# Kernel optimization log

Hardware: AMD Instinct MI355X
Metric: run time of the kernel (lower is better)

The kernel has to match this reference:

```python
import jax, jax.numpy as jnp
import numpy as np
from jax import lax

# Static problem dims (match input_specs)
B, N, F, H, C = 128, 512, 512, 256, 10
EPG = 8192            # edges per graph
K1, K2 = 256, 128      # pooling_ratio=0.5 applied twice
LAMB = 1.0
BN_EPS = 1e-5


def setup_inputs() -> dict:
    key = jax.random.key(0)
    ks = jax.random.split(key, 24)
    x = jax.random.normal(ks[0], (B * N, F), dtype=jnp.float32)
    offs = (jnp.arange(B, dtype=jnp.int32) * N)[:, None]
    src = jax.random.randint(ks[1], (B, EPG), 0, N, dtype=jnp.int32) + offs
    dst = jax.random.randint(ks[2], (B, EPG), 0, N, dtype=jnp.int32) + offs
    edge_index = jnp.stack([src.reshape(-1), dst.reshape(-1)])
    batch = jnp.repeat(jnp.arange(B, dtype=jnp.int32), N)
    s = 0.05
    p = {
        'W1': jax.random.normal(ks[3], (F, H)) * s, 'b1': jnp.zeros((H,)),
        'W2': jax.random.normal(ks[4], (H, H)) * s, 'b2': jnp.zeros((H,)),
        'W3': jax.random.normal(ks[5], (H, H)) * s, 'b3': jnp.zeros((H,)),
        'att1': jax.random.normal(ks[6], (H, 2)) * s,
        'att2': jax.random.normal(ks[7], (H, 2)) * s,
        'bn_gamma': jnp.ones((H,)), 'bn_beta': jnp.zeros((H,)),
        'bn_mean': jnp.zeros((H,)), 'bn_var': jnp.ones((H,)),
        'lin1_w': jax.random.normal(ks[8], (2 * H, H)) * s, 'lin1_b': jnp.zeros((H,)),
        'lin2_w': jax.random.normal(ks[9], (H, H // 2)) * s, 'lin2_b': jnp.zeros((H // 2,)),
        'lin3_w': jax.random.normal(ks[10], (H // 2, C)) * s, 'lin3_b': jnp.zeros((C,)),
    }
    return {'x': x, 'edge_index': edge_index, 'batch': batch, **p}


def gcn_sparse(x, src, dst, W, b):
    """GCNConv: D^-1/2 (A+I) D^-1/2 X W + b over an edge list."""
    n = x.shape[0]
    loop = jnp.arange(n, dtype=src.dtype)
    s = jnp.concatenate([src, loop])
    d = jnp.concatenate([dst, loop])
    deg = jax.ops.segment_sum(jnp.ones_like(d, jnp.float32), d, num_segments=n)
    dinv = lax.rsqrt(jnp.maximum(deg, 1.0))
    xw = x @ W
    msg = xw[s] * (dinv[s] * dinv[d])[:, None]
    return jax.ops.segment_sum(msg, d, num_segments=n) + b


def structure_learn(x_sel, A_ind, att):
    # GAT-style additive attention over all node pairs within each pooled graph,
    # biased by lamb * induced adjacency, row-softmax normalized (dense HGPSL path).
    e = x_sel @ att[:, 0]              # [B,k]
    f = x_sel @ att[:, 1]              # [B,k]
    logits = e[:, :, None] + f[:, None, :] + LAMB * A_ind
    return jax.nn.softmax(logits, axis=-1)


def pool_sparse(x, src, dst, att, k_out):
    """HGPSL pool on the sparse input graph -> dense pooled graphs [B,k,k]."""
    n = x.shape[0]
    deg = jnp.maximum(jax.ops.segment_sum(jnp.ones_like(dst, jnp.float32), dst, num_segments=n), 1.0)
    neigh = jax.ops.segment_sum(x[src], dst, num_segments=n)
    score = jnp.abs(x - neigh / deg[:, None]).sum(-1)          # node information score ||(I - D^-1 A)X||_1
    _, idx = lax.top_k(score.reshape(B, N), k_out)              # [B,k]
    offs = (jnp.arange(B, dtype=jnp.int32) * N)[:, None]
    perm = (idx.astype(jnp.int32) + offs).reshape(-1)
    x_sel = x[perm].reshape(B, k_out, -1)
    # induced adjacency among selected nodes (scatter into k+1 dummy slot)
    rank = jnp.full((B * N,), -1, jnp.int32).at[perm].set(jnp.tile(jnp.arange(k_out, dtype=jnp.int32), B))
    g = src // N
    ns, nd = rank[src], rank[dst]
    valid = (ns >= 0) & (nd >= 0)
    A = jnp.zeros((B, k_out + 1, k_out + 1), jnp.float32)
    A = A.at[g, jnp.where(valid, ns, k_out), jnp.where(valid, nd, k_out)].set(1.0)
    A_ind = A[:, :k_out, :k_out]
    return x_sel, structure_learn(x_sel, A_ind, att)


def pool_dense(x, adj, att, k_out):
    deg = jnp.maximum(adj.sum(-1), 1e-9)
    prop = jnp.einsum('bij,bjf->bif', adj, x) / deg[..., None]
    score = jnp.abs(x - prop).sum(-1)                           # [B,k_in]
    _, idx = lax.top_k(score, k_out)
    x_sel = jnp.take_along_axis(x, idx[:, :, None], axis=1)
    A_ind = jax.vmap(lambda a, i: a[i][:, i])(adj, idx)
    return x_sel, structure_learn(x_sel, A_ind, att)


def gcn_dense(x, adj, W, b):
    k = x.shape[1]
    A = adj + jnp.eye(k, dtype=x.dtype)
    dinv = lax.rsqrt(A.sum(-1))
    An = A * dinv[:, :, None] * dinv[:, None, :]
    return jnp.einsum('bij,bjf->bif', An, x @ W) + b


def readout(x):
    # [gmp || gap] over nodes of each graph
    return jnp.concatenate([x.max(axis=1), x.mean(axis=1)], axis=-1)


def reference(x, edge_index, batch, W1, b1, W2, b2, W3, b3, att1, att2,
              bn_gamma, bn_beta, bn_mean, bn_var,
              lin1_w, lin1_b, lin2_w, lin2_b, lin3_w, lin3_b):
    src, dst = edge_index[0], edge_index[1]
    h = jax.nn.relu(gcn_sparse(x, src, dst, W1, b1))            # conv1, [B*N, H]
    x__ = h
    h1, adj1 = pool_sparse(h, src, dst, att1, K1)                # pool1 -> [B,K1,H]
    x1 = readout(h1)
    hb = (h1 - bn_mean) * lax.rsqrt(bn_var + BN_EPS) * bn_gamma + bn_beta  # BN (eval)
    h2 = jax.nn.relu(gcn_dense(hb, adj1, W2, b2))                # conv2
    h2, adj2 = pool_dense(h2, adj1, att2, K2)                    # pool2 -> [B,K2,H]
    x2 = readout(h2)
    h3 = jax.nn.relu(gcn_dense(h2, adj2, W3, b3))                # conv3
    x3 = readout(h3)
    g = jax.nn.relu(x1) + jax.nn.relu(x2) + jax.nn.relu(x3)      # [B, 2H]
    g = jax.nn.relu(g @ lin1_w + lin1_b)                         # dropout=identity (eval)
    g = jax.nn.relu(g @ lin2_w + lin2_b)
    x_ = g
    logp = jax.nn.log_softmax(g @ lin3_w + lin3_b, axis=-1)
    return (x_, logp, x__)
```

## Files before the change

kernel.cpp:

```cpp
#include <hip/hip_runtime.h>
#include <stdint.h>


#define B_   128
#define N_   512
#define NN_  65536
#define E_   1048576
#define LAMB_ 1.0f

typedef unsigned short ushort_t;
typedef __attribute__((ext_vector_type(8))) short bf16x8;
typedef __attribute__((ext_vector_type(8))) unsigned short u16x8;
typedef __attribute__((ext_vector_type(4))) float f32x4;

__device__ inline float waveReduceSum(float v) {
    #pragma unroll
    for (int o = 32; o > 0; o >>= 1) v += __shfl_down(v, o, 64);
    return v;
}

__device__ inline ushort_t f2bf(float f) {
    unsigned u = __float_as_uint(f);
    u += 0x7fffu + ((u >> 16) & 1u);
    return (ushort_t)(u >> 16);
}

__global__ void split_w_kernel(const float* __restrict__ W, ushort_t* __restrict__ Whi,
                               ushort_t* __restrict__ Wlo) {
    int k = blockIdx.x;
    int n = threadIdx.x;
    float w = W[k * 256 + n];
    ushort_t h = f2bf(w);
    float hf = __uint_as_float((unsigned)h << 16);
    ushort_t l = f2bf(w - hf);
    Whi[n * 512 + k] = h;
    Wlo[n * 512 + k] = l;
}

__global__ __launch_bounds__(256) void gemm_xw_mfma(
    const float* __restrict__ A, const ushort_t* __restrict__ Bhi,
    const ushort_t* __restrict__ Blo, float* __restrict__ C) {
    int m0 = blockIdx.x * 128, n0 = blockIdx.y * 128;
    __shared__ __align__(16) ushort_t As[2][4][128][8];
    int tid = threadIdx.x;
    int lane = tid & 63, w = tid >> 6;
    int wm = (w & 1) * 64, wn = (w >> 1) * 64;
    int fl = lane & 15, fh = lane >> 4;
    f32x4 acc[4][4] = {};
    int sm = tid >> 1, sk = (tid & 1) * 16;
    const float* Ap = A + (size_t)(m0 + sm) * 512 + sk;
    float4 p0 = *(const float4*)(Ap + 0);
    float4 p1 = *(const float4*)(Ap + 4);
    float4 p2 = *(const float4*)(Ap + 8);
    float4 p3 = *(const float4*)(Ap + 12);
    for (int ks = 0; ks < 16; ks++) {
        float f0[8] = {p0.x, p0.y, p0.z, p0.w, p1.x, p1.y, p1.z, p1.w};
        float f1[8] = {p2.x, p2.y, p2.z, p2.w, p3.x, p3.y, p3.z, p3.w};
        u16x8 h0, h1, l0, l1;
        #pragma unroll
        for (int i = 0; i < 8; i++) {
            unsigned u = __float_as_uint(f0[i]);
            unsigned rh = u + 0x7fffu + ((u >> 16) & 1u);
            ushort_t hh = (ushort_t)(rh >> 16);
            float lf = f0[i] - __uint_as_float((unsigned)hh << 16);
            unsigned ul = __float_as_uint(lf);
            unsigned rl = ul + 0x7fffu + ((ul >> 16) & 1u);
            h0[i] = hh;
            l0[i] = (ushort_t)(rl >> 16);
        }
        #pragma unroll
        for (int i = 0; i < 8; i++) {
            unsigned u = __float_as_uint(f1[i]);
            unsigned rh = u + 0x7fffu + ((u >> 16) & 1u);
            ushort_t hh = (ushort_t)(rh >> 16);
            float lf = f1[i] - __uint_as_float((unsigned)hh << 16);
            unsigned ul = __float_as_uint(lf);
            unsigned rl = ul + 0x7fffu + ((ul >> 16) & 1u);
            h1[i] = hh;
            l1[i] = (ushort_t)(rl >> 16);
        }
        __syncthreads();
        int khi = sk >> 3;
        *(u16x8*)&As[0][khi][sm][0]     = h0;
        *(u16x8*)&As[0][khi + 1][sm][0] = h1;
        *(u16x8*)&As[1][khi][sm][0]     = l0;
        *(u16x8*)&As[1][khi + 1][sm][0] = l1;
        __syncthreads();
        if (ks < 15) {
            Ap += 32;
            p0 = *(const float4*)(Ap + 0);
            p1 = *(const float4*)(Ap + 4);
            p2 = *(const float4*)(Ap + 8);
            p3 = *(const float4*)(Ap + 12);
        }
        bf16x8 ah[4], al[4], bh[4], bl[4];
        #pragma unroll
        for (int mi = 0; mi < 4; mi++) {
            ah[mi] = *(const bf16x8*)&As[0][fh][wm + mi * 16 + fl][0];
            al[mi] = *(const bf16x8*)&As[1][fh][wm + mi * 16 + fl][0];
        }
        int kg = ks * 32 + fh * 8;
        #pragma unroll
        for (int ni = 0; ni < 4; ni++) {
            size_t boff = (size_t)(n0 + wn + ni * 16 + fl) * 512 + kg;
            bh[ni] = *(const bf16x8*)&Bhi[boff];
            bl[ni] = *(const bf16x8*)&Blo[boff];
        }
        #pragma unroll
        for (int mi = 0; mi < 4; mi++)
            #pragma unroll
            for (int ni = 0; ni < 4; ni++) {
                acc[mi][ni] = __builtin_amdgcn_mfma_f32_16x16x32_bf16(al[mi], bh[ni], acc[mi][ni], 0, 0, 0);
                acc[mi][ni] = __builtin_amdgcn_mfma_f32_16x16x32_bf16(ah[mi], bl[ni], acc[mi][ni], 0, 0, 0);
                acc[mi][ni] = __builtin_amdgcn_mfma_f32_16x16x32_bf16(ah[mi], bh[ni], acc[mi][ni], 0, 0, 0);
            }
    }
    #pragma unroll
    for (int mi = 0; mi < 4; mi++)
        #pragma unroll
        for (int ni = 0; ni < 4; ni++)
            #pragma unroll
            for (int r = 0; r < 4; r++)
                C[(size_t)(m0 + wm + mi * 16 + fh * 4 + r) * 256 + n0 + wn + ni * 16 + fl]
                    = acc[mi][ni][r];
}

__global__ void count_kernel(const int* __restrict__ dst, int* __restrict__ indeg) {
    int e = blockIdx.x * 256 + threadIdx.x;
    if (e < E_) atomicAdd(&indeg[dst[e] & 65535], 1);
}
__global__ void scan_kernel(const int* __restrict__ indeg, int* __restrict__ rowstart,
                            int* __restrict__ cursor) {
    __shared__ int part[1024];
    int t = threadIdx.x;
    int base = t * 64;
    int s = 0;
    for (int i = 0; i < 64; i++) s += indeg[base + i];
    part[t] = s;
    __syncthreads();
    for (int off = 1; off < 1024; off <<= 1) {
        int v = (t >= off) ? part[t - off] : 0;
        __syncthreads();
        part[t] += v;
        __syncthreads();
    }
    int run = (t == 0) ? 0 : part[t - 1];
    for (int i = 0; i < 64; i++) {
        rowstart[base + i] = run;
        cursor[base + i] = run;
        run += indeg[base + i];
    }
}
__global__ void scatter_csr_kernel(const int* __restrict__ src, const int* __restrict__ dst,
                                   int* __restrict__ cursor, int* __restrict__ csr) {
    int e = blockIdx.x * 256 + threadIdx.x;
    if (e < E_) {
        int pos = atomicAdd(&cursor[dst[e] & 65535], 1);
        csr[pos & (E_ - 1)] = src[e] & 65535;
    }
}
__global__ void dinv_kernel(const int* __restrict__ indeg, float* __restrict__ dinv) {
    int i = blockIdx.x * 256 + threadIdx.x;
    dinv[i] = rsqrtf((float)indeg[i] + 1.0f);
}

__global__ void aggregate_kernel(const float4* __restrict__ xw, const int* __restrict__ rowstart,
                                 const int* __restrict__ indeg, const float* __restrict__ dinv,
                                 const int* __restrict__ csr, const float* __restrict__ b1,
                                 float4* __restrict__ hout) {
    int bid = (blockIdx.x & 7) * 2048 + (blockIdx.x >> 3);
    int node = bid * 4 + (threadIdx.x >> 6);
    int lane = threadIdx.x & 63;
    int beg = rowstart[node], cnt = indeg[node];
    float di = dinv[node];
    float4 acc = make_float4(0.f, 0.f, 0.f, 0.f);
    for (int t = 0; t < cnt; t++) {
        int s = csr[(beg + t) & (E_ - 1)] & 65535;
        float w = dinv[s] * di;
        float4 v = xw[(size_t)s * 64 + lane];
        acc.x += v.x * w; acc.y += v.y * w; acc.z += v.z * w; acc.w += v.w * w;
    }
    {
        float w = di * di;
        float4 v = xw[(size_t)node * 64 + lane];
        acc.x += v.x * w; acc.y += v.y * w; acc.z += v.z * w; acc.w += v.w * w;
    }
    int c4 = lane * 4;
    acc.x = fmaxf(acc.x + b1[c4 + 0], 0.f);
    acc.y = fmaxf(acc.y + b1[c4 + 1], 0.f);
    acc.z = fmaxf(acc.z + b1[c4 + 2], 0.f);
    acc.w = fmaxf(acc.w + b1[c4 + 3], 0.f);
    hout[(size_t)node * 64 + lane] = acc;
}

__global__ void score_kernel(const float4* __restrict__ h, const int* __restrict__ rowstart,
                             const int* __restrict__ indeg, const int* __restrict__ csr,
                             float* __restrict__ score) {
    int bid = (blockIdx.x & 7) * 2048 + (blockIdx.x >> 3);
    int node = bid * 4 + (threadIdx.x >> 6);
    int lane = threadIdx.x & 63;
    int beg = rowstart[node], cnt = indeg[node];
    float degp = fmaxf((float)cnt, 1.0f);
    float4 nb = make_float4(0.f, 0.f, 0.f, 0.f);
    for (int t = 0; t < cnt; t++) {
        int s = csr[(beg + t) & (E_ - 1)] & 65535;
        float4 v = h[(size_t)s * 64 + lane];
        nb.x += v.x; nb.y += v.y; nb.z += v.z; nb.w += v.w;
    }
    float4 x = h[(size_t)node * 64 + lane];
    float p = fabsf(x.x - nb.x / degp) + fabsf(x.y - nb.y / degp) +
              fabsf(x.z - nb.z / degp) + fabsf(x.w - nb.w / degp);
    p = waveReduceSum(p);
    if (lane == 0) score[node] = p;
}

__global__ void topk_kernel(const float* __restrict__ score, int n, int k,
                            int* __restrict__ out_local, int* __restrict__ rank, int Nfull) {
    int b = blockIdx.x, i = threadIdx.x;
    __shared__ float ss[512];
    __shared__ int si[512];
    ss[i] = score[b * n + i];
    si[i] = i;
    __syncthreads();
    for (int kk = 2; kk <= n; kk <<= 1)
        for (int j = kk >> 1; j > 0; j >>= 1) {
            int l = i ^ j;
            if (l > i) {
                float s1 = ss[i], s2 = ss[l];
                int i1 = si[i], i2 = si[l];
                bool up = ((i & kk) == 0);
                bool before = (s1 > s2) || (s1 == s2 && i1 < i2);
                bool doswap = up ? (!before) : before;
                if (doswap) { ss[i] = s2; ss[l] = s1; si[i] = i2; si[l] = i1; }
            }
            __syncthreads();
        }
    if (i < k) {
        int loc = si[i];
        out_local[b * k + i] = loc;
        if (rank) rank[b * Nfull + loc] = i;
    }
}

__global__ void gather_rows_kernel(const float4* __restrict__ src, const int* __restrict__ idxl,
                                   int k, int Nfull, float4* __restrict__ dstp) {
    int row = blockIdx.x;
    int b = row / k;
    int node = b * Nfull + (idxl[row] & (Nfull - 1));
    dstp[(size_t)row * 64 + threadIdx.x] = src[(size_t)node * 64 + threadIdx.x];
}
__global__ void readout_kernel(const float* __restrict__ x, int k, float* __restrict__ out) {
    int b = blockIdx.x, q = blockIdx.y, c = threadIdx.x;
    int chunk = k >> 2;
    int j0 = q * chunk;
    float mx = 0.f, sm = 0.f;
    for (int j = j0; j < j0 + chunk; j++) {
        float v = x[((size_t)(b * k + j)) * 256 + c];
        mx = fmaxf(mx, v);
        sm += v;
    }
    atomicMax((unsigned int*)&out[b * 512 + c], __float_as_uint(mx));
    atomicAdd(&out[b * 512 + 256 + c], sm * (1.0f / (float)k));
}
__global__ void readout_idx_kernel(const float* __restrict__ x, const int* __restrict__ idx,
                                   int k, int Nfull, float* __restrict__ out) {
    int b = blockIdx.x, q = blockIdx.y, c = threadIdx.x;
    int chunk = k >> 2;
    int j0 = q * chunk;
    float mx = 0.f, sm = 0.f;
    for (int j = j0; j < j0 + chunk; j++) {
        int node = b * Nfull + (idx[b * k + j] & (Nfull - 1));
        float v = x[(size_t)node * 256 + c];
        mx = fmaxf(mx, v);
        sm += v;
    }
    atomicMax((unsigned int*)&out[b * 512 + c], __float_as_uint(mx));
    atomicAdd(&out[b * 512 + 256 + c], sm * (1.0f / (float)k));
}
__global__ void ef_plain_kernel(const float4* __restrict__ x, const float* __restrict__ att,
                                float* __restrict__ e, float* __restrict__ f) {
    int row = blockIdx.x * 4 + (threadIdx.x >> 6);
    int lane = threadIdx.x & 63;
    float4 v = x[(size_t)row * 64 + lane];
    const float* ap = att + lane * 8;
    float es = v.x * ap[0] + v.y * ap[2] + v.z * ap[4] + v.w * ap[6];
    float fs = v.x * ap[1] + v.y * ap[3] + v.z * ap[5] + v.w * ap[7];
    es = waveReduceSum(es);
    fs = waveReduceSum(fs);
    if (lane == 0) { e[row] = es; f[row] = fs; }
}
__global__ void ef_idx_kernel(const float4* __restrict__ x, const int* __restrict__ idx,
                              int k, int Nfull, const float* __restrict__ att,
                              float* __restrict__ e, float* __restrict__ f) {
    int row = blockIdx.x * 4 + (threadIdx.x >> 6);
    int lane = threadIdx.x & 63;
    int b = row / k;
    int node = b * Nfull + (idx[row] & (Nfull - 1));
    float4 v = x[(size_t)node * 64 + lane];
    const float* ap = att + lane * 8;
    float es = v.x * ap[0] + v.y * ap[2] + v.z * ap[4] + v.w * ap[6];
    float fs = v.x * ap[1] + v.y * ap[3] + v.z * ap[5] + v.w * ap[7];
    es = waveReduceSum(es);
    fs = waveReduceSum(fs);
    if (lane == 0) { e[row] = es; f[row] = fs; }
}

__global__ void scatter_A_kernel(const int* __restrict__ src, const int* __restrict__ dst,
                                 const int* __restrict__ rank, float* __restrict__ adj1) {
    int e = blockIdx.x * 256 + threadIdx.x;
    if (e >= E_) return;
    int s = src[e] & 65535, d = dst[e] & 65535;
    int ns = rank[s], nd = rank[d];
    if ((unsigned)ns < 256u && (unsigned)nd < 256u) {
        int g = s >> 9;
        adj1[(size_t)g * 65536 + ns * 256 + nd] = 1.0f;
    }
}
__global__ void softmax_adj_kernel(float* __restrict__ adj, const float* __restrict__ e,
                                   const float* __restrict__ f, int k) {
    int row = blockIdx.x;
    int b = row / k;
    int c = threadIdx.x;
    __shared__ float red[256];
    float v = adj[(size_t)row * k + c];
    float lg = e[row] + f[b * k + c] + LAMB_ * v;
    red[c] = lg;
    __syncthreads();
    for (int s = k >> 1; s > 0; s >>= 1) {
        if (c < s) red[c] = fmaxf(red[c], red[c + s]);
        __syncthreads();
    }
    float mx = red[0];
    __syncthreads();
    float ex = expf(lg - mx);
    red[c] = ex;
    __syncthreads();
    for (int s = k >> 1; s > 0; s >>= 1) {
        if (c < s) red[c] += red[c + s];
        __syncthreads();
    }
    adj[(size_t)row * k + c] = ex / red[0];
}
__global__ void rowsum_kernel(const float* __restrict__ adj, int k,
                              float* __restrict__ rowsum, float* __restrict__ dinv) {
    int row = blockIdx.x * 4 + (threadIdx.x >> 6);
    int lane = threadIdx.x & 63;
    float s = 0.f;
    for (int c = lane; c < k; c += 64) s += adj[(size_t)row * k + c];
    s = waveReduceSum(s);
    if (lane == 0) { rowsum[row] = s; dinv[row] = rsqrtf(s + 1.0f); }
}
__global__ void gather_adj2_kernel(const float* __restrict__ adj1, const int* __restrict__ idx2,
                                   float* __restrict__ adj2) {
    int ii = blockIdx.x, b = blockIdx.y, jj = threadIdx.x;
    int ri = idx2[b * 128 + ii] & 255, rj = idx2[b * 128 + jj] & 255;
    adj2[((size_t)(b * 128 + ii)) * 128 + jj] = adj1[(size_t)b * 65536 + ri * 256 + rj];
}
__global__ void bn_kernel(const float* g, const float* be,
                          const float* me, const float* va,
                          float* sBN, float* tBN) {
    int c = threadIdx.x;
    float s = g[c] * rsqrtf(va[c] + 1e-5f);
    sBN[c] = s;
    tBN[c] = be[c] - me[c] * s;
}

#define GEMM_PROLOG \
    int b = blockIdx.z; \
    int m0 = blockIdx.x * 64, n0 = blockIdx.y * 64; \
    __shared__ float As[16 * 68], Bs[16 * 68]; \
    int tid = threadIdx.x, tx = tid & 15, ty = tid >> 4; \
    float acc[4][4] = {{0.f}}; \
    (void)b;

#define GEMM_INNER \
    __syncthreads(); \
    _Pragma("unroll") \
    for (int kk = 0; kk < 16; kk++) { \
        float4 a = *(const float4*)&As[kk * 68 + ty * 4]; \
        float4 bv = *(const float4*)&Bs[kk * 68 + tx * 4]; \
        float av[4] = {a.x, a.y, a.z, a.w}; \
        float bb[4] = {bv.x, bv.y, bv.z, bv.w}; \
        _Pragma("unroll") \
        for (int i2 = 0; i2 < 4; i2++) \
            _Pragma("unroll") \
            for (int j2 = 0; j2 < 4; j2++) acc[i2][j2] += av[i2] * bb[j2]; \
    }

__global__ __launch_bounds__(256) void gemm_x2_kernel(
    const float* __restrict__ H1, const float* __restrict__ W2,
    const float* __restrict__ sBN, const float* __restrict__ tBN,
    const float* __restrict__ dinv1, float* __restrict__ X2) {
    GEMM_PROLOG
    const float* A = H1 + (size_t)b * 65536;
    for (int k0 = 0; k0 < 256; k0 += 16) {
        __syncthreads();
        #pragma unroll
        for (int i = 0; i < 4; i++) {
            int idx = tid + i * 256;
            int kk = idx & 15, m = idx >> 4;
            As[kk * 68 + m] = A[(m0 + m) * 256 + k0 + kk] * sBN[k0 + kk] + tBN[k0 + kk];
        }
        #pragma unroll
        for (int i = 0; i < 4; i++) {
            int idx = tid + i * 256;
            int n = idx & 63, kk = idx >> 6;
            Bs[kk * 68 + n] = W2[(k0 + kk) * 256 + n0 + n];
        }
        GEMM_INNER
    }
    #pragma unroll
    for (int i = 0; i < 4; i++) {
        int row = m0 + ty * 4 + i;
        float dv = dinv1[b * 256 + row];
        #pragma unroll
        for (int j = 0; j < 4; j++)
            X2[(size_t)b * 65536 + row * 256 + n0 + tx * 4 + j] = acc[i][j] * dv;
    }
}

__global__ __launch_bounds__(256) void gemm_h2_kernel(
    const float* __restrict__ ADJ1, const float* __restrict__ X2,
    const float* __restrict__ dinv1, const float* __restrict__ b2,
    float* __restrict__ H2) {
    GEMM_PROLOG
    const float* A = ADJ1 + (size_t)b * 65536;
    const float* Bp = X2 + (size_t)b * 65536;
    for (int k0 = 0; k0 < 256; k0 += 16) {
        __syncthreads();
        #pragma unroll
        for (int i = 0; i < 4; i++) {
            int idx = tid + i * 256;
            int kk = idx & 15, m = idx >> 4;
            As[kk * 68 + m] = A[(m0 + m) * 256 + k0 + kk];
        }
        #pragma unroll
        for (int i = 0; i < 4; i++) {
            int idx = tid + i * 256;
            int n = idx & 63, kk = idx >> 6;
            Bs[kk * 68 + n] = Bp[(k0 + kk) * 256 + n0 + n];
        }
        GEMM_INNER
    }
    #pragma unroll
    for (int i = 0; i < 4; i++) {
        int row = m0 + ty * 4 + i;
        float dv = dinv1[b * 256 + row];
        #pragma unroll
        for (int j = 0; j < 4; j++) {
            int col = n0 + tx * 4 + j;
            float v = (acc[i][j] + X2[(size_t)b * 65536 + row * 256 + col]) * dv + b2[col];
            H2[(size_t)b * 65536 + row * 256 + col] = fmaxf(v, 0.f);
        }
    }
}

__global__ __launch_bounds__(256) void gemm_score_kernel(
    const float* __restrict__ ADJ1, const float* __restrict__ H2,
    const float* __restrict__ rowsum1, float* __restrict__ score2) {
    GEMM_PROLOG
    const float* A = ADJ1 + (size_t)b * 65536;
    const float* Bp = H2 + (size_t)b * 65536;
    for (int k0 = 0; k0 < 256; k0 += 16) {
        __syncthreads();
        #pragma unroll
        for (int i = 0; i < 4; i++) {
            int idx = tid + i * 256;
            int kk = idx & 15, m = idx >> 4;
            As[kk * 68 + m] = A[(m0 + m) * 256 + k0 + kk];
        }
        #pragma unroll
        for (int i = 0; i < 4; i++) {
            int idx = tid + i * 256;
            int n = idx & 63, kk = idx >> 6;
            Bs[kk * 68 + n] = Bp[(k0 + kk) * 256 + n0 + n];
        }
        GEMM_INNER
    }
    float rpart[4];
    #pragma unroll
    for (int i = 0; i < 4; i++) {
        int row = m0 + ty * 4 + i;
        float deg = fmaxf(rowsum1[b * 256 + row], 1e-9f);
        float s = 0.f;
        #pragma unroll
        for (int j = 0; j < 4; j++) {
            int col = n0 + tx * 4 + j;
            s += fabsf(H2[(size_t)b * 65536 + row * 256 + col] - acc[i][j] / deg);
        }
        rpart[i] = s;
    }
    __syncthreads();
    #pragma unroll
    for (int i = 0; i < 4; i++) As[(ty * 4 + i) * 17 + tx] = rpart[i];
    __syncthreads();
    if (tid < 64) {
        float s = 0.f;
        #pragma unroll
        for (int x = 0; x < 16; x++) s += As[tid * 17 + x];
        atomicAdd(&score2[b * 256 + m0 + tid], s);
    }
}

__global__ __launch_bounds__(256) void gemm_x3_kernel(
    const float* __restrict__ H2, const int* __restrict__ idx2,
    const float* __restrict__ W3,
    const float* __restrict__ dinv2, float* __restrict__ X3) {
    GEMM_PROLOG
    __shared__ int rowsS[64];
    if (tid < 64) rowsS[tid] = b * 256 + (idx2[b * 128 + m0 + tid] & 255);
    for (int k0 = 0; k0 < 256; k0 += 16) {
        __syncthreads();
        #pragma unroll
        for (int i = 0; i < 4; i++) {
            int idx = tid + i * 256;
            int kk = idx & 15, m = idx >> 4;
            As[kk * 68 + m] = H2[(size_t)rowsS[m] * 256 + k0 + kk];
        }
        #pragma unroll
        for (int i = 0; i < 4; i++) {
            int idx = tid + i * 256;
            int n = idx & 63, kk = idx >> 6;
            Bs[kk * 68 + n] = W3[(k0 + kk) * 256 + n0 + n];
        }
        GEMM_INNER
    }
    #pragma unroll
    for (int i = 0; i < 4; i++) {
        int row = m0 + ty * 4 + i;
        float dv = dinv2[b * 128 + row];
        #pragma unroll
        for (int j = 0; j < 4; j++)
            X3[(size_t)b * 32768 + row * 256 + n0 + tx * 4 + j] = acc[i][j] * dv;
    }
}

__global__ __launch_bounds__(256) void gemm_h3_kernel(
    const float* __restrict__ ADJ2, const float* __restrict__ X3,
    const float* __restrict__ dinv2, const float* __restrict__ b3,
    float* __restrict__ H3) {
    GEMM_PROLOG
    const float* A = ADJ2 + (size_t)b * 16384;
    const float* Bp = X3 + (size_t)b * 32768;
    for (int k0 = 0; k0 < 128; k0 += 16) {
        __syncthreads();
        #pragma unroll
        for (int i = 0; i < 4; i++) {
            int idx = tid + i * 256;
            int kk = idx & 15, m = idx >> 4;
            As[kk * 68 + m] = A[(m0 + m) * 128 + k0 + kk];
        }
        #pragma unroll
        for (int i = 0; i < 4; i++) {
            int idx = tid + i * 256;
            int n = idx & 63, kk = idx >> 6;
            Bs[kk * 68 + n] = Bp[(k0 + kk) * 256 + n0 + n];
        }
        GEMM_INNER
    }
    #pragma unroll
    for (int i = 0; i < 4; i++) {
        int row = m0 + ty * 4 + i;
        float dv = dinv2[b * 128 + row];
        #pragma unroll
        for (int j = 0; j < 4; j++) {
            int col = n0 + tx * 4 + j;
            float v = (acc[i][j] + X3[(size_t)b * 32768 + row * 256 + col]) * dv + b3[col];
            H3[(size_t)b * 32768 + row * 256 + col] = fmaxf(v, 0.f);
        }
    }
}

__global__ void head_kernel(const float* __restrict__ x1, const float* __restrict__ x2,
                            const float* __restrict__ x3,
                            const float* __restrict__ w1, const float* __restrict__ b1,
                            const float* __restrict__ w2, const float* __restrict__ b2,
                            const float* __restrict__ w3, const float* __restrict__ b3,
                            float* __restrict__ out_x, float* __restrict__ out_lp) {
    int b = blockIdx.x, t = threadIdx.x;
    __shared__ float g[512], g1[256], g2[128], lg[10];
    __shared__ float lse;
    for (int i = t; i < 512; i += 256)
        g[i] = fmaxf(x1[b * 512 + i], 0.f) + fmaxf(x2[b * 512 + i], 0.f) + fmaxf(x3[b * 512 + i], 0.f);
    __syncthreads();
    {
        float acc = b1[t];
        for (int kk = 0; kk < 512; kk++) acc += g[kk] * w1[kk * 256 + t];
        g1[t] = fmaxf(acc, 0.f);
    }
    __syncthreads();
    if (t < 128) {
        float acc = b2[t];
        for (int kk = 0; kk < 256; kk++) acc += g1[kk] * w2[kk * 128 + t];
        float r = fmaxf(acc, 0.f);
        g2[t] = r;
        out_x[b * 128 + t] = r;
    }
    __syncthreads();
    if (t < 10) {
        float acc = b3[t];
        for (int kk = 0; kk < 128; kk++) acc += g2[kk] * w3[kk * 10 + t];
        lg[t] = acc;
    }
    __syncthreads();
    if (t == 0) {
        float m = -1e30f;
        for (int i = 0; i < 10; i++) m = fmaxf(m, lg[i]);
        float s = 0.f;
        for (int i = 0; i < 10; i++) s += expf(lg[i] - m);
        lse = m + logf(s);
    }
    __syncthreads();
    if (t < 10) out_lp[b * 10 + t] = lg[t] - lse;
}

extern "C" void kernel_launch(void* const* d_in, const int* in_sizes, int n_in,
                              void* d_out, int out_size, void* d_ws, size_t ws_size,
                              hipStream_t stream) {
    const float* X    = (const float*)d_in[0];
    const int*   EI   = (const int*)d_in[1];
    const float* W1   = (const float*)d_in[3];
    const float* B1v  = (const float*)d_in[4];
    const float* W2   = (const float*)d_in[5];
    const float* B2v  = (const float*)d_in[6];
    const float* W3   = (const float*)d_in[7];
    const float* B3v  = (const float*)d_in[8];
    const float* ATT1 = (const float*)d_in[9];
    const float* ATT2 = (const float*)d_in[10];
    const float* GAM  = (const float*)d_in[11];
    const float* BET  = (const float*)d_in[12];
    const float* MEA  = (const float*)d_in[13];
    const float* VAR  = (const float*)d_in[14];
    const float* L1W  = (const float*)d_in[15];
    const float* L1B  = (const float*)d_in[16];
    const float* L2W  = (const float*)d_in[17];
    const float* L2B  = (const float*)d_in[18];
    const float* L3W  = (const float*)d_in[19];
    const float* L3B  = (const float*)d_in[20];
    float* OUT = (float*)d_out;
    const int OFF_LOGP = 16384, OFF_XU = 17664;

    const int* src = EI;
    const int* dst = EI + E_;

    uint8_t* w = (uint8_t*)d_ws;
    const size_t MB = 1u << 20;
    float* XWp  = (float*)(w + 0);
    float* ADJ1 = (float*)(w + 0);
    float* X2   = (float*)(w + 32 * MB);
    float* X3   = (float*)(w + 32 * MB);
    float* H3   = (float*)(w + 48 * MB);
    int*   CSR    = (int*)(w + 68 * MB);
    int*   INDEG  = (int*)(w + 72 * MB);
    int*   RSTART = INDEG + 65536;
    int*   CURSOR = RSTART + 65536;
    float* DINV   = (float*)(CURSOR + 65536);
    float* SCORE  = (float*)(w + 73 * MB);
    float* H1   = (float*)(w + 76 * MB);
    float* H2   = H1;
    float* ADJ2 = (float*)(w + 108 * MB);
    uint8_t* mp = w + 116 * MB;
    int*   RANK   = (int*)mp;   mp += 256 * 1024;
    int*   IDX1   = (int*)mp;   mp += 128 * 1024;
    int*   IDX2   = (int*)mp;   mp += 64 * 1024;
    float* E1     = (float*)mp; mp += 128 * 1024;
    float* F1     = (float*)mp; mp += 128 * 1024;
    float* E2     = (float*)mp; mp += 64 * 1024;
    float* F2     = (float*)mp; mp += 64 * 1024;
    float* RS1    = (float*)mp; mp += 128 * 1024;
    float* DV1    = (float*)mp; mp += 128 * 1024;
    float* RS2    = (float*)mp; mp += 64 * 1024;
    float* DV2    = (float*)mp; mp += 64 * 1024;
    float* SC2    = (float*)mp; mp += 128 * 1024;
    float* SBN    = (float*)mp; mp += 4 * 1024;
    float* TBN    = (float*)mp; mp += 4 * 1024;
    float* X1R    = (float*)mp; mp += 256 * 1024;
    float* X2R    = (float*)mp; mp += 256 * 1024;
    float* X3R    = (float*)mp; mp += 256 * 1024;
    ushort_t* WHI = (ushort_t*)mp; mp += 256 * 1024;
    ushort_t* WLO = (ushort_t*)mp; mp += 256 * 1024;

    float* Hout = OUT + OFF_XU;

    hipMemsetAsync(INDEG, 0, 256 * 1024, stream);
    hipMemsetAsync(RANK, 0xFF, 256 * 1024, stream);
    hipMemsetAsync(SC2, 0, 128 * 1024, stream);
    hipMemsetAsync(X1R, 0, 768 * 1024, stream);

    split_w_kernel<<<512, 256, 0, stream>>>(W1, WHI, WLO);
    gemm_xw_mfma<<<dim3(512, 2), 256, 0, stream>>>(X, WHI, WLO, XWp);
    count_kernel<<<4096, 256, 0, stream>>>(dst, INDEG);
    scan_kernel<<<1, 1024, 0, stream>>>(INDEG, RSTART, CURSOR);
    scatter_csr_kernel<<<4096, 256, 0, stream>>>(src, dst, CURSOR, CSR);
    dinv_kernel<<<256, 256, 0, stream>>>(INDEG, DINV);
    aggregate_kernel<<<16384, 256, 0, stream>>>((const float4*)XWp, RSTART, INDEG, DINV,
                                                CSR, B1v, (float4*)Hout);
    score_kernel<<<16384, 256, 0, stream>>>((const float4*)Hout, RSTART, INDEG, CSR, SCORE);
    topk_kernel<<<128, 512, 0, stream>>>(SCORE, 512, 256, IDX1, RANK, 512);
    gather_rows_kernel<<<32768, 64, 0, stream>>>((const float4*)Hout, IDX1, 256, 512, (float4*)H1);
    readout_kernel<<<dim3(128, 4), 256, 0, stream>>>(H1, 256, X1R);
    ef_plain_kernel<<<8192, 256, 0, stream>>>((const float4*)H1, ATT1, E1, F1);
    hipMemsetAsync(ADJ1, 0, (size_t)32 * MB, stream);
    scatter_A_kernel<<<4096, 256, 0, stream>>>(src, dst, RANK, ADJ1);
    softmax_adj_kernel<<<32768, 256, 0, stream>>>(ADJ1, E1, F1, 256);
    rowsum_kernel<<<8192, 256, 0, stream>>>(ADJ1, 256, RS1, DV1);
    bn_kernel<<<1, 256, 0, stream>>>(GAM, BET, MEA, VAR, SBN, TBN);
    gemm_x2_kernel<<<dim3(4, 4, 128), 256, 0, stream>>>(H1, W2, SBN, TBN, DV1, X2);
    gemm_h2_kernel<<<dim3(4, 4, 128), 256, 0, stream>>>(ADJ1, X2, DV1, B2v, H2);
    gemm_score_kernel<<<dim3(4, 4, 128), 256, 0, stream>>>(ADJ1, H2, RS1, SC2);
    topk_kernel<<<128, 256, 0, stream>>>(SC2, 256, 128, IDX2, nullptr, 0);
    readout_idx_kernel<<<dim3(128, 4), 256, 0, stream>>>(H2, IDX2, 128, 256, X2R);
    ef_idx_kernel<<<4096, 256, 0, stream>>>((const float4*)H2, IDX2, 128, 256, ATT2, E2, F2);
    gather_adj2_kernel<<<dim3(128, 128), 128, 0, stream>>>(ADJ1, IDX2, ADJ2);
    softmax_adj_kernel<<<16384, 128, 0, stream>>>(ADJ2, E2, F2, 128);
    rowsum_kernel<<<4096, 256, 0, stream>>>(ADJ2, 128, RS2, DV2);
    gemm_x3_kernel<<<dim3(2, 4, 128), 256, 0, stream>>>(H2, IDX2, W3, DV2, X3);
    gemm_h3_kernel<<<dim3(2, 4, 128), 256, 0, stream>>>(ADJ2, X3, DV2, B3v, H3);
    readout_kernel<<<dim3(128, 4), 256, 0, stream>>>(H3, 128, X3R);
    head_kernel<<<128, 256, 0, stream>>>(X1R, X2R, X3R, L1W, L1B, L2W, L2B, L3W, L3B,
                                         OUT, OUT + OFF_LOGP);
}
```

Before: 1.049 ms.

## Move dense GCN and score GEMMs to split-bf16 MFMA with transposed intermediates

Replaces the FP32 shared-memory SIMT GEMMs for conv2, the pool2 score and conv3 with MFMA kernels. Each operand is split into hi/lo bf16 halves and multiplied with three MFMAs to keep near-fp32 accuracy. Intermediates (softmaxed adjacencies, BN-applied H1, X2/H2/X3) are now produced directly as hi/lo bf16 in transposed layouts by the upstream kernels, and BN is fused into the row gather. The goal is to cut the FP32 FMA cost of the batched dense GEMMs, at the price of loading operands straight from global memory without LDS staging and of some extra split/convert work plus a reshuffled workspace layout.

```diff
diff --git a/kernel.cpp b/kernel.cpp
--- a/kernel.cpp
+++ b/kernel.cpp
@@ -18,23 +18,80 @@
     for (int o = 32; o > 0; o >>= 1) v += __shfl_down(v, o, 64);
     return v;
 }
-
 __device__ inline ushort_t f2bf(float f) {
     unsigned u = __float_as_uint(f);
     u += 0x7fffu + ((u >> 16) & 1u);
     return (ushort_t)(u >> 16);
 }
-
-__global__ void split_w_kernel(const float* __restrict__ W, ushort_t* __restrict__ Whi,
-                               ushort_t* __restrict__ Wlo) {
+__device__ inline void split2(float f, ushort_t& h, ushort_t& l) {
+    h = f2bf(f);
+    float r = f - __uint_as_float((unsigned)h << 16);
+    l = f2bf(r);
+}
+__device__ inline float bfu(ushort_t s) { return __uint_as_float((unsigned)s << 16); }
+
+__device__ inline void store_T4(ushort_t* __restrict__ Th, ushort_t* __restrict__ Tl,
+                                size_t base, const float* v) {
+    ushort_t h[4], l[4];
+    #pragma unroll
+    for (int r = 0; r < 4; r++) split2(v[r], h[r], l[r]);
+    uint2 ph = make_uint2((unsigned)h[0] | ((unsigned)h[1] << 16),
+                          (unsigned)h[2] | ((unsigned)h[3] << 16));
+    uint2 pl = make_uint2((unsigned)l[0] | ((unsigned)l[1] << 16),
+                          (unsigned)l[2] | ((unsigned)l[3] << 16));
+    *(uint2*)&Th[base] = ph;
+    *(uint2*)&Tl[base] = pl;
+}
+__device__ inline void load_T4(const ushort_t* __restrict__ Th, const ushort_t* __restrict__ Tl,
+                               size_t base, float* v) {
+    uint2 ph = *(const uint2*)&Th[base];
+    uint2 pl = *(const uint2*)&Tl[base];
+    v[0] = __uint_as_float(ph.x << 16) + __uint_as_float(pl.x << 16);
+    v[1] = __uint_as_float(ph.x & 0xffff0000u) + __uint_as_float(pl.x & 0xffff0000u);
+    v[2] = __uint_as_float(ph.y << 16) + __uint_as_float(pl.y << 16);
+    v[3] = __uint_as_float(ph.y & 0xffff0000u) + __uint_as_float(pl.y & 0xffff0000u);
+}
+
+template<int KSTEPS>
+__device__ __attribute__((always_inline)) void mfma_core(
+    const ushort_t* __restrict__ Ah, const ushort_t* __restrict__ Al, int lda,
+    const ushort_t* __restrict__ Bh, const ushort_t* __restrict__ Bl, int ldb,
+    int rowbase, int colbase, int fl, int fh, f32x4 acc[4][4]) {
+    #pragma unroll
+    for (int ks = 0; ks < KSTEPS; ks++) {
+        int kg = ks * 32 + fh * 8;
+        bf16x8 bh[4], bl[4];
+        #pragma unroll
+        for (int ni = 0; ni < 4; ni++) {
+            size_t off = (size_t)(colbase + ni * 16 + fl) * ldb + kg;
+            bh[ni] = *(const bf16x8*)&Bh[off];
+            bl[ni] = *(const bf16x8*)&Bl[off];
+        }
+        #pragma unroll
+        for (int mi = 0; mi < 4; mi++) {
+            size_t off = (size_t)(rowbase + mi * 16 + fl) * lda + kg;
+            bf16x8 ah = *(const bf16x8*)&Ah[off];
+            bf16x8 al = *(const bf16x8*)&Al[off];
+            #pragma unroll
+            for (int ni = 0; ni < 4; ni++) {
+                acc[mi][ni] = __builtin_amdgcn_mfma_f32_16x16x32_bf16(al, bh[ni], acc[mi][ni], 0, 0, 0);
+                acc[mi][ni] = __builtin_amdgcn_mfma_f32_16x16x32_bf16(ah, bl[ni], acc[mi][ni], 0, 0, 0);
+                acc[mi][ni] = __builtin_amdgcn_mfma_f32_16x16x32_bf16(ah, bh[ni], acc[mi][ni], 0, 0, 0);
+            }
+        }
+    }
+}
+
+__global__ void split_wT_kernel(const float* __restrict__ W, int Kd,
+                                ushort_t* __restrict__ Whi, ushort_t* __restrict__ Wlo) {
     int k = blockIdx.x;
     int n = threadIdx.x;
-    float w = W[k * 256 + n];
-    ushort_t h = f2bf(w);
-    float hf = __uint_as_float((unsigned)h << 16);
-    ushort_t l = f2bf(w - hf);
-    Whi[n * 512 + k] = h;
-    Wlo[n * 512 + k] = l;
+    int Nn = blockDim.x;
+    float w = W[k * Nn + n];
+    ushort_t h, l;
+    split2(w, h, l);
+    Whi[n * Kd + k] = h;
+    Wlo[n * Kd + k] = l;
 }
 
 __global__ __launch_bounds__(256) void gemm_xw_mfma(
@@ -59,25 +116,15 @@
         u16x8 h0, h1, l0, l1;
         #pragma unroll
         for (int i = 0; i < 8; i++) {
-            unsigned u = __float_as_uint(f0[i]);
-            unsigned rh = u + 0x7fffu + ((u >> 16) & 1u);
-            ushort_t hh = (ushort_t)(rh >> 16);
-            float lf = f0[i] - __uint_as_float((unsigned)hh << 16);
-            unsigned ul = __float_as_uint(lf);
-            unsigned rl = ul + 0x7fffu + ((ul >> 16) & 1u);
-            h0[i] = hh;
-            l0[i] = (ushort_t)(rl >> 16);
+            ushort_t hh, ll;
+            split2(f0[i], hh, ll);
+            h0[i] = hh; l0[i] = ll;
         }
         #pragma unroll
         for (int i = 0; i < 8; i++) {
-            unsigned u = __float_as_uint(f1[i]);
-            unsigned rh = u + 0x7fffu + ((u >> 16) & 1u);
-            ushort_t hh = (ushort_t)(rh >> 16);
-            float lf = f1[i] - __uint_as_float((unsigned)hh << 16);
-            unsigned ul = __float_as_uint(lf);
-            unsigned rl = ul + 0x7fffu + ((ul >> 16) & 1u);
-            h1[i] = hh;
-            l1[i] = (ushort_t)(rl >> 16);
+            ushort_t hh, ll;
+            split2(f1[i], hh, ll);
+            h1[i] = hh; l1[i] = ll;
         }
         __syncthreads();
         int khi = sk >> 3;
@@ -242,13 +289,33 @@
     }
 }
 
-__global__ void gather_rows_kernel(const float4* __restrict__ src, const int* __restrict__ idxl,
-                                   int k, int Nfull, float4* __restrict__ dstp) {
+__global__ void gather_bn_kernel(const float4* __restrict__ src, const int* __restrict__ idxl,
+                                 const float* __restrict__ sBN, const float* __restrict__ tBN,
+                                 float4* __restrict__ H1, ushort_t* __restrict__ BNh,
+                                 ushort_t* __restrict__ BNl) {
     int row = blockIdx.x;
-    int b = row / k;
-    int node = b * Nfull + (idxl[row] & (Nfull - 1));
-    dstp[(size_t)row * 64 + threadIdx.x] = src[(size_t)node * 64 + threadIdx.x];
-}
+    int b = row >> 8;
+    int node = b * 512 + (idxl[row] & 511);
+    int lane = threadIdx.x;
+    float4 v = src[(size_t)node * 64 + lane];
+    H1[(size_t)row * 64 + lane] = v;
+    int c0 = lane * 4;
+    float bn[4];
+    bn[0] = v.x * sBN[c0 + 0] + tBN[c0 + 0];
+    bn[1] = v.y * sBN[c0 + 1] + tBN[c0 + 1];
+    bn[2] = v.z * sBN[c0 + 2] + tBN[c0 + 2];
+    bn[3] = v.w * sBN[c0 + 3] + tBN[c0 + 3];
+    ushort_t h[4], l[4];
+    #pragma unroll
+    for (int j = 0; j < 4; j++) split2(bn[j], h[j], l[j]);
+    uint2 ph = make_uint2((unsigned)h[0] | ((unsigned)h[1] << 16),
+                          (unsigned)h[2] | ((unsigned)h[3] << 16));
+    uint2 pl = make_uint2((unsigned)l[0] | ((unsigned)l[1] << 16),
+                          (unsigned)l[2] | ((unsigned)l[3] << 16));
+    *(uint2*)&BNh[(size_t)row * 256 + c0] = ph;
+    *(uint2*)&BNl[(size_t)row * 256 + c0] = pl;
+}
+
 __global__ void readout_kernel(const float* __restrict__ x, int k, float* __restrict__ out) {
     int b = blockIdx.x, q = blockIdx.y, c = threadIdx.x;
     int chunk = k >> 2;
@@ -262,15 +329,16 @@
     atomicMax((unsigned int*)&out[b * 512 + c], __float_as_uint(mx));
     atomicAdd(&out[b * 512 + 256 + c], sm * (1.0f / (float)k));
 }
-__global__ void readout_idx_kernel(const float* __restrict__ x, const int* __restrict__ idx,
-                                   int k, int Nfull, float* __restrict__ out) {
+__global__ void readout_split_kernel(const ushort_t* __restrict__ Ah,
+                                     const ushort_t* __restrict__ Al,
+                                     int k, float* __restrict__ out) {
     int b = blockIdx.x, q = blockIdx.y, c = threadIdx.x;
     int chunk = k >> 2;
     int j0 = q * chunk;
     float mx = 0.f, sm = 0.f;
     for (int j = j0; j < j0 + chunk; j++) {
-        int node = b * Nfull + (idx[b * k + j] & (Nfull - 1));
-        float v = x[(size_t)node * 256 + c];
+        size_t idx = ((size_t)(b * k + j)) * 256 + c;
+        float v = bfu(Ah[idx]) + bfu(Al[idx]);
         mx = fmaxf(mx, v);
         sm += v;
     }
@@ -289,17 +357,17 @@
     fs = waveReduceSum(fs);
     if (lane == 0) { e[row] = es; f[row] = fs; }
 }
-__global__ void ef_idx_kernel(const float4* __restrict__ x, const int* __restrict__ idx,
-                              int k, int Nfull, const float* __restrict__ att,
-                              float* __restrict__ e, float* __restrict__ f) {
+__global__ void ef_split_kernel(const ushort_t* __restrict__ Ah, const ushort_t* __restrict__ Al,
+                                const float* __restrict__ att,
+                                float* __restrict__ e, float* __restrict__ f) {
     int row = blockIdx.x * 4 + (threadIdx.x >> 6);
     int lane = threadIdx.x & 63;
-    int b = row / k;
-    int node = b * Nfull + (idx[row] & (Nfull - 1));
-    float4 v = x[(size_t)node * 64 + lane];
+    size_t base = (size_t)row * 256 + lane * 4;
+    float v[4];
+    load_T4(Ah, Al, base, v);
     const float* ap = att + lane * 8;
-    float es = v.x * ap[0] + v.y * ap[2] + v.z * ap[4] + v.w * ap[6];
-    float fs = v.x * ap[1] + v.y * ap[3] + v.z * ap[5] + v.w * ap[7];
+    float es = v[0] * ap[0] + v[1] * ap[2] + v[2] * ap[4] + v[3] * ap[6];
+    float fs = v[0] * ap[1] + v[1] * ap[3] + v[2] * ap[5] + v[3] * ap[7];
     es = waveReduceSum(es);
     fs = waveReduceSum(fs);
     if (lane == 0) { e[row] = es; f[row] = fs; }
@@ -316,13 +384,14 @@
         adj1[(size_t)g * 65536 + ns * 256 + nd] = 1.0f;
     }
 }
-__global__ void softmax_adj_kernel(float* __restrict__ adj, const float* __restrict__ e,
-                                   const float* __restrict__ f, int k) {
+__global__ void softmax_split_kernel(const float* __restrict__ ind, const float* __restrict__ e,
+                                     const float* __restrict__ f, int k,
+                                     ushort_t* __restrict__ oh, ushort_t* __restrict__ ol) {
     int row = blockIdx.x;
     int b = row / k;
     int c = threadIdx.x;
     __shared__ float red[256];
-    float v = adj[(size_t)row * k + c];
+    float v = ind[(size_t)row * k + c];
     float lg = e[row] + f[b * k + c] + LAMB_ * v;
     red[c] = lg;
     __syncthreads();
@@ -339,22 +408,33 @@
         if (c < s) red[c] += red[c + s];
         __syncthreads();
     }
-    adj[(size_t)row * k + c] = ex / red[0];
-}
-__global__ void rowsum_kernel(const float* __restrict__ adj, int k,
-                              float* __restrict__ rowsum, float* __restrict__ dinv) {
+    float p = ex / red[0];
+    ushort_t h, l;
+    split2(p, h, l);
+    oh[(size_t)row * k + c] = h;
+    ol[(size_t)row * k + c] = l;
+}
+__global__ void rowsum_split_kernel(const ushort_t* __restrict__ Ah,
+                                    const ushort_t* __restrict__ Al, int k,
+                                    float* __restrict__ rowsum, float* __restrict__ dinv) {
     int row = blockIdx.x * 4 + (threadIdx.x >> 6);
     int lane = threadIdx.x & 63;
     float s = 0.f;
-    for (int c = lane; c < k; c += 64) s += adj[(size_t)row * k + c];
+    for (int c = lane; c < k; c += 64) {
+        size_t idx = (size_t)row * k + c;
+        s += bfu(Ah[idx]) + bfu(Al[idx]);
+    }
     s = waveReduceSum(s);
     if (lane == 0) { rowsum[row] = s; dinv[row] = rsqrtf(s + 1.0f); }
 }
-__global__ void gather_adj2_kernel(const float* __restrict__ adj1, const int* __restrict__ idx2,
-                                   float* __restrict__ adj2) {
+__global__ void gather_adj2_split_kernel(const ushort_t* __restrict__ Ah,
+                                         const ushort_t* __restrict__ Al,
+                                         const int* __restrict__ idx2,
+                                         float* __restrict__ adj2) {
     int ii = blockIdx.x, b = blockIdx.y, jj = threadIdx.x;
     int ri = idx2[b * 128 + ii] & 255, rj = idx2[b * 128 + jj] & 255;
-    adj2[((size_t)(b * 128 + ii)) * 128 + jj] = adj1[(size_t)b * 65536 + ri * 256 + rj];
+    size_t idx = (size_t)b * 65536 + ri * 256 + rj;
+    adj2[((size_t)(b * 128 + ii)) * 128 + jj] = bfu(Ah[idx]) + bfu(Al[idx]);
 }
 __global__ void bn_kernel(const float* g, const float* be,
                           const float* me, const float* va,
@@ -365,208 +445,199 @@
     tBN[c] = be[c] - me[c] * s;
 }
 
-#define GEMM_PROLOG \
-    int b = blockIdx.z; \
-    int m0 = blockIdx.x * 64, n0 = blockIdx.y * 64; \
-    __shared__ float As[16 * 68], Bs[16 * 68]; \
-    int tid = threadIdx.x, tx = tid & 15, ty = tid >> 4; \
-    float acc[4][4] = {{0.f}}; \
-    (void)b;
-
-#define GEMM_INNER \
-    __syncthreads(); \
-    _Pragma("unroll") \
-    for (int kk = 0; kk < 16; kk++) { \
-        float4 a = *(const float4*)&As[kk * 68 + ty * 4]; \
-        float4 bv = *(const float4*)&Bs[kk * 68 + tx * 4]; \
-        float av[4] = {a.x, a.y, a.z, a.w}; \
-        float bb[4] = {bv.x, bv.y, bv.z, bv.w}; \
-        _Pragma("unroll") \
-        for (int i2 = 0; i2 < 4; i2++) \
-            _Pragma("unroll") \
-            for (int j2 = 0; j2 < 4; j2++) acc[i2][j2] += av[i2] * bb[j2]; \
-    }
-
-__global__ __launch_bounds__(256) void gemm_x2_kernel(
-    const float* __restrict__ H1, const float* __restrict__ W2,
-    const float* __restrict__ sBN, const float* __restrict__ tBN,
-    const float* __restrict__ dinv1, float* __restrict__ X2) {
-    GEMM_PROLOG
-    const float* A = H1 + (size_t)b * 65536;
-    for (int k0 = 0; k0 < 256; k0 += 16) {
-        __syncthreads();
-        #pragma unroll
-        for (int i = 0; i < 4; i++) {
-            int idx = tid + i * 256;
-            int kk = idx & 15, m = idx >> 4;
-            As[kk * 68 + m] = A[(m0 + m) * 256 + k0 + kk] * sBN[k0 + kk] + tBN[k0 + kk];
-        }
-        #pragma unroll
-        for (int i = 0; i < 4; i++) {
-            int idx = tid + i * 256;
-            int n = idx & 63, kk = idx >> 6;
-            Bs[kk * 68 + n] = W2[(k0 + kk) * 256 + n0 + n];
-        }
-        GEMM_INNER
-    }
-    #pragma unroll
-    for (int i = 0; i < 4; i++) {
-        int row = m0 + ty * 4 + i;
-        float dv = dinv1[b * 256 + row];
-        #pragma unroll
-        for (int j = 0; j < 4; j++)
-            X2[(size_t)b * 65536 + row * 256 + n0 + tx * 4 + j] = acc[i][j] * dv;
-    }
-}
-
-__global__ __launch_bounds__(256) void gemm_h2_kernel(
-    const float* __restrict__ ADJ1, const float* __restrict__ X2,
+__global__ void gather_a3_kernel(const ushort_t* __restrict__ H2Th,
+                                 const ushort_t* __restrict__ H2Tl,
+                                 const int* __restrict__ idx2,
+                                 ushort_t* __restrict__ A3h, ushort_t* __restrict__ A3l) {
+    int row = blockIdx.x;
+    int b = row >> 7;
+    int node = idx2[row] & 255;
+    int lane = threadIdx.x;
+    int c0 = lane * 4;
+    unsigned h[4], l[4];
+    #pragma unroll
+    for (int j = 0; j < 4; j++) {
+        size_t idx = ((size_t)(b * 256 + c0 + j)) * 256 + node;
+        h[j] = H2Th[idx];
+        l[j] = H2Tl[idx];
+    }
+    uint2 ph = make_uint2(h[0] | (h[1] << 16), h[2] | (h[3] << 16));
+    uint2 pl = make_uint2(l[0] | (l[1] << 16), l[2] | (l[3] << 16));
+    *(uint2*)&A3h[(size_t)row * 256 + c0] = ph;
+    *(uint2*)&A3l[(size_t)row * 256 + c0] = pl;
+}
+
+__global__ __launch_bounds__(256) void gemm_x2_mfma(
+    const ushort_t* __restrict__ Ah, const ushort_t* __restrict__ Al,
+    const ushort_t* __restrict__ Bh, const ushort_t* __restrict__ Bl,
+    const float* __restrict__ dinv1,
+    ushort_t* __restrict__ XTh, ushort_t* __restrict__ XTl) {
+    int b = blockIdx.z;
+    int m0 = blockIdx.x * 128, n0 = blockIdx.y * 128;
+    int lane = threadIdx.x & 63, w = threadIdx.x >> 6;
+    int wm = (w & 1) * 64, wn = (w >> 1) * 64;
+    int fl = lane & 15, fh = lane >> 4;
+    f32x4 acc[4][4] = {};
+    mfma_core<8>(Ah + (size_t)b * 65536, Al + (size_t)b * 65536, 256,
+                 Bh, Bl, 256, m0 + wm, n0 + wn, fl, fh, acc);
+    #pragma unroll
+    for (int mi = 0; mi < 4; mi++) {
+        int row0 = m0 + wm + mi * 16 + fh * 4;
+        float4 dv = *(const float4*)&dinv1[b * 256 + row0];
+        float dvv[4] = {dv.x, dv.y, dv.z, dv.w};
+        #pragma unroll
+        for (int ni = 0; ni < 4; ni++) {
+            int col = n0 + wn + ni * 16 + fl;
+            float v[4];
+            #pragma unroll
+            for (int r = 0; r < 4; r++) v[r] = acc[mi][ni][r] * dvv[r];
+            store_T4(XTh, XTl, ((size_t)(b * 256 + col)) * 256 + row0, v);
+        }
+    }
+}
+
+__global__ __launch_bounds__(256) void gemm_h2_mfma(
+    const ushort_t* __restrict__ Ah, const ushort_t* __restrict__ Al,
+    const ushort_t* __restrict__ Xh, const ushort_t* __restrict__ Xl,
     const float* __restrict__ dinv1, const float* __restrict__ b2,
-    float* __restrict__ H2) {
-    GEMM_PROLOG
-    const float* A = ADJ1 + (size_t)b * 65536;
-    const float* Bp = X2 + (size_t)b * 65536;
-    for (int k0 = 0; k0 < 256; k0 += 16) {
-        __syncthreads();
-        #pragma unroll
-        for (int i = 0; i < 4; i++) {
-            int idx = tid + i * 256;
-            int kk = idx & 15, m = idx >> 4;
-            As[kk * 68 + m] = A[(m0 + m) * 256 + k0 + kk];
-        }
-        #pragma unroll
-        for (int i = 0; i < 4; i++) {
-            int idx = tid + i * 256;
-            int n = idx & 63, kk = idx >> 6;
-            Bs[kk * 68 + n] = Bp[(k0 + kk) * 256 + n0 + n];
-        }
-        GEMM_INNER
-    }
-    #pragma unroll
-    for (int i = 0; i < 4; i++) {
-        int row = m0 + ty * 4 + i;
-        float dv = dinv1[b * 256 + row];
-        #pragma unroll
-        for (int j = 0; j < 4; j++) {
-            int col = n0 + tx * 4 + j;
-            float v = (acc[i][j] + X2[(size_t)b * 65536 + row * 256 + col]) * dv + b2[col];
-            H2[(size_t)b * 65536 + row * 256 + col] = fmaxf(v, 0.f);
-        }
-    }
-}
-
-__global__ __launch_bounds__(256) void gemm_score_kernel(
-    const float* __restrict__ ADJ1, const float* __restrict__ H2,
+    ushort_t* __restrict__ Hh, ushort_t* __restrict__ Hl) {
+    int b = blockIdx.z;
+    int m0 = blockIdx.x * 128, n0 = blockIdx.y * 128;
+    int lane = threadIdx.x & 63, w = threadIdx.x >> 6;
+    int wm = (w & 1) * 64, wn = (w >> 1) * 64;
+    int fl = lane & 15, fh = lane >> 4;
+    f32x4 acc[4][4] = {};
+    mfma_core<8>(Ah + (size_t)b * 65536, Al + (size_t)b * 65536, 256,
+                 Xh + (size_t)b * 65536, Xl + (size_t)b * 65536, 256,
+                 m0 + wm, n0 + wn, fl, fh, acc);
+    #pragma unroll
+    for (int mi = 0; mi < 4; mi++) {
+        int row0 = m0 + wm + mi * 16 + fh * 4;
+        float4 dv = *(const float4*)&dinv1[b * 256 + row0];
+        float dvv[4] = {dv.x, dv.y, dv.z, dv.w};
+        #pragma unroll
+        for (int ni = 0; ni < 4; ni++) {
+            int col = n0 + wn + ni * 16 + fl;
+            size_t baseT = ((size_t)(b * 256 + col)) * 256 + row0;
+            float xv[4], v[4];
+            load_T4(Xh, Xl, baseT, xv);
+            float bc = b2[col];
+            #pragma unroll
+            for (int r = 0; r < 4; r++)
+                v[r] = fmaxf((acc[mi][ni][r] + xv[r]) * dvv[r] + bc, 0.f);
+            store_T4(Hh, Hl, baseT, v);
+        }
+    }
+}
+
+__global__ __launch_bounds__(256) void gemm_score_mfma(
+    const ushort_t* __restrict__ Ah, const ushort_t* __restrict__ Al,
+    const ushort_t* __restrict__ Hh, const ushort_t* __restrict__ Hl,
     const float* __restrict__ rowsum1, float* __restrict__ score2) {
-    GEMM_PROLOG
-    const float* A = ADJ1 + (size_t)b * 65536;
-    const float* Bp = H2 + (size_t)b * 65536;
-    for (int k0 = 0; k0 < 256; k0 += 16) {
-        __syncthreads();
-        #pragma unroll
-        for (int i = 0; i < 4; i++) {
-            int idx = tid + i * 256;
-            int kk = idx & 15, m = idx >> 4;
-            As[kk * 68 + m] = A[(m0 + m) * 256 + k0 + kk];
-        }
-        #pragma unroll
-        for (int i = 0; i < 4; i++) {
-            int idx = tid + i * 256;
-            int n = idx & 63, kk = idx >> 6;
-            Bs[kk * 68 + n] = Bp[(k0 + kk) * 256 + n0 + n];
-        }
-        GEMM_INNER
-    }
-    float rpart[4];
-    #pragma unroll
-    for (int i = 0; i < 4; i++) {
-        int row = m0 + ty * 4 + i;
-        float deg = fmaxf(rowsum1[b * 256 + row], 1e-9f);
-        float s = 0.f;
-        #pragma unroll
-        for (int j = 0; j < 4; j++) {
-            int col = n0 + tx * 4 + j;
-            s += fabsf(H2[(size_t)b * 65536 + row * 256 + col] - acc[i][j] / deg);
-        }
-        rpart[i] = s;
-    }
-    __syncthreads();
-    #pragma unroll
-    for (int i = 0; i < 4; i++) As[(ty * 4 + i) * 17 + tx] = rpart[i];
-    __syncthreads();
-    if (tid < 64) {
-        float s = 0.f;
-        #pragma unroll
-        for (int x = 0; x < 16; x++) s += As[tid * 17 + x];
-        atomicAdd(&score2[b * 256 + m0 + tid], s);
-    }
-}
-
-__global__ __launch_bounds__(256) void gemm_x3_kernel(
-    const float* __restrict__ H2, const int* __restrict__ idx2,
-    const float* __restrict__ W3,
-    const float* __restrict__ dinv2, float* __restrict__ X3) {
-    GEMM_PROLOG
-    __shared__ int rowsS[64];
-    if (tid < 64) rowsS[tid] = b * 256 + (idx2[b * 128 + m0 + tid] & 255);
-    for (int k0 = 0; k0 < 256; k0 += 16) {
-        __syncthreads();
-        #pragma unroll
-        for (int i = 0; i < 4; i++) {
-            int idx = tid + i * 256;
-            int kk = idx & 15, m = idx >> 4;
-            As[kk * 68 + m] = H2[(size_t)rowsS[m] * 256 + k0 + kk];
-        }
-        #pragma unroll
-        for (int i = 0; i < 4; i++) {
-            int idx = tid + i * 256;
-            int n = idx & 63, kk = idx >> 6;
-            Bs[kk * 68 + n] = W3[(k0 + kk) * 256 + n0 + n];
-        }
-        GEMM_INNER
-    }
-    #pragma unroll
-    for (int i = 0; i < 4; i++) {
-        int row = m0 + ty * 4 + i;
-        float dv = dinv2[b * 128 + row];
-        #pragma unroll
-        for (int j = 0; j < 4; j++)
-            X3[(size_t)b * 32768 + row * 256 + n0 + tx * 4 + j] = acc[i][j] * dv;
-    }
-}
-
-__global__ __launch_bounds__(256) void gemm_h3_kernel(
-    const float* __restrict__ ADJ2, const float* __restrict__ X3,
+    int b = blockIdx.z;
+    int m0 = blockIdx.x * 128, n0 = blockIdx.y * 128;
+    int lane = threadIdx.x & 63, w = threadIdx.x >> 6;
+    int wm = (w & 1) * 64, wn = (w >> 1) * 64;
+    int fl = lane & 15, fh = lane >> 4;
+    f32x4 acc[4][4] = {};
+    mfma_core<8>(Ah + (size_t)b * 65536, Al + (size_t)b * 65536, 256,
+                 Hh + (size_t)b * 65536, Hl + (size_t)b * 65536, 256,
+                 m0 + wm, n0 + wn, fl, fh, acc);
+    float part[4][4];
+    #pragma unroll
+    for (int mi = 0; mi < 4; mi++)
+        #pragma unroll
+        for (int r = 0; r < 4; r++) part[mi][r] = 0.f;
+    #pragma unroll
+    for (int mi = 0; mi < 4; mi++) {
+        int row0 = m0 + wm + mi * 16 + fh * 4;
+        float4 rs = *(const float4*)&rowsum1[b * 256 + row0];
+        float rd[4] = {1.0f / fmaxf(rs.x, 1e-9f), 1.0f / fmaxf(rs.y, 1e-9f),
+                       1.0f / fmaxf(rs.z, 1e-9f), 1.0f / fmaxf(rs.w, 1e-9f)};
+        #pragma unroll
+        for (int ni = 0; ni < 4; ni++) {
+            int col = n0 + wn + ni * 16 + fl;
+            size_t baseT = ((size_t)(b * 256 + col)) * 256 + row0;
+            float hv[4];
+            load_T4(Hh, Hl, baseT, hv);
+            #pragma unroll
+            for (int r = 0; r < 4; r++)
+                part[mi][r] += fabsf(hv[r] - acc[mi][ni][r] * rd[r]);
+        }
+    }
+    #pragma unroll
+    for (int mi = 0; mi < 4; mi++) {
+        int row0 = m0 + wm + mi * 16 + fh * 4;
+        #pragma unroll
+        for (int r = 0; r < 4; r++) {
+            float s = part[mi][r];
+            #pragma unroll
+            for (int o = 8; o >= 1; o >>= 1) s += __shfl_xor(s, o, 64);
+            if (fl == 0) atomicAdd(&score2[b * 256 + row0 + r], s);
+        }
+    }
+}
+
+__global__ __launch_bounds__(256) void gemm_x3_mfma(
+    const ushort_t* __restrict__ Ah, const ushort_t* __restrict__ Al,
+    const ushort_t* __restrict__ Bh, const ushort_t* __restrict__ Bl,
+    const float* __restrict__ dinv2,
+    ushort_t* __restrict__ XTh, ushort_t* __restrict__ XTl) {
+    int b = blockIdx.z;
+    int m0 = blockIdx.x * 128, n0 = blockIdx.y * 128;
+    int lane = threadIdx.x & 63, w = threadIdx.x >> 6;
+    int wm = (w & 1) * 64, wn = (w >> 1) * 64;
+    int fl = lane & 15, fh = lane >> 4;
+    f32x4 acc[4][4] = {};
+    mfma_core<8>(Ah + (size_t)b * 32768, Al + (size_t)b * 32768, 256,
+                 Bh, Bl, 256, m0 + wm, n0 + wn, fl, fh, acc);
+    #pragma unroll
+    for (int mi = 0; mi < 4; mi++) {
+        int row0 = m0 + wm + mi * 16 + fh * 4;
+        float4 dv = *(const float4*)&dinv2[b * 128 + row0];
+        float dvv[4] = {dv.x, dv.y, dv.z, dv.w};
+        #pragma unroll
+        for (int ni = 0; ni < 4; ni++) {
+            int col = n0 + wn + ni * 16 + fl;
+            float v[4];
+            #pragma unroll
+            for (int r = 0; r < 4; r++) v[r] = acc[mi][ni][r] * dvv[r];
+            store_T4(XTh, XTl, ((size_t)(b * 256 + col)) * 128 + row0, v);
+        }
+    }
+}
+
+__global__ __launch_bounds__(256) void gemm_h3_mfma(
+    const ushort_t* __restrict__ Ah, const ushort_t* __restrict__ Al,
+    const ushort_t* __restrict__ Xh, const ushort_t* __restrict__ Xl,
     const float* __restrict__ dinv2, const float* __restrict__ b3,
     float* __restrict__ H3) {
-    GEMM_PROLOG
-    const float* A = ADJ2 + (size_t)b * 16384;
-    const float* Bp = X3 + (size_t)b * 32768;
-    for (int k0 = 0; k0 < 128; k0 += 16) {
-        __syncthreads();
-        #pragma unroll
-        for (int i = 0; i < 4; i++) {
-            int idx = tid + i * 256;
-            int kk = idx & 15, m = idx >> 4;
-            As[kk * 68 + m] = A[(m0 + m) * 128 + k0 + kk];
-        }
-        #pragma unroll
-        for (int i = 0; i < 4; i++) {
-            int idx = tid + i * 256;
-            int n = idx & 63, kk = idx >> 6;
-            Bs[kk * 68 + n] = Bp[(k0 + kk) * 256 + n0 + n];
-        }
-        GEMM_INNER
-    }
-    #pragma unroll
-    for (int i = 0; i < 4; i++) {
-        int row = m0 + ty * 4 + i;
-        float dv = dinv2[b * 128 + row];
-        #pragma unroll
-        for (int j = 0; j < 4; j++) {
-            int col = n0 + tx * 4 + j;
-            float v = (acc[i][j] + X3[(size_t)b * 32768 + row * 256 + col]) * dv + b3[col];
-            H3[(size_t)b * 32768 + row * 256 + col] = fmaxf(v, 0.f);
+    int b = blockIdx.z;
+    int m0 = blockIdx.x * 128, n0 = blockIdx.y * 128;
+    int lane = threadIdx.x & 63, w = threadIdx.x >> 6;
+    int wm = (w & 1) * 64, wn = (w >> 1) * 64;
+    int fl = lane & 15, fh = lane >> 4;
+    f32x4 acc[4][4] = {};
+    mfma_core<4>(Ah + (size_t)b * 16384, Al + (size_t)b * 16384, 128,
+                 Xh + (size_t)b * 32768, Xl + (size_t)b * 32768, 128,
+                 m0 + wm, n0 + wn, fl, fh, acc);
+    #pragma unroll
+    for (int mi = 0; mi < 4; mi++) {
+        int row0 = m0 + wm + mi * 16 + fh * 4;
+        float4 dv = *(const float4*)&dinv2[b * 128 + row0];
+        float dvv[4] = {dv.x, dv.y, dv.z, dv.w};
+        #pragma unroll
+        for (int ni = 0; ni < 4; ni++) {
+            int col = n0 + wn + ni * 16 + fl;
+            size_t baseT = ((size_t)(b * 256 + col)) * 128 + row0;
+            float xv[4];
+            load_T4(Xh, Xl, baseT, xv);
+            float bc = b3[col];
+            #pragma unroll
+            for (int r = 0; r < 4; r++) {
+                float v = fmaxf((acc[mi][ni][r] + xv[r]) * dvv[r] + bc, 0.f);
+                H3[(size_t)b * 32768 + (size_t)(row0 + r) * 256 + col] = v;
+            }
         }
     }
 }
@@ -645,21 +716,32 @@
 
     uint8_t* w = (uint8_t*)d_ws;
     const size_t MB = 1u << 20;
-    float* XWp  = (float*)(w + 0);
-    float* ADJ1 = (float*)(w + 0);
-    float* X2   = (float*)(w + 32 * MB);
-    float* X3   = (float*)(w + 32 * MB);
-    float* H3   = (float*)(w + 48 * MB);
-    int*   CSR    = (int*)(w + 68 * MB);
-    int*   INDEG  = (int*)(w + 72 * MB);
+    float*    XWp     = (float*)(w + 0);
+    float*    IND1    = (float*)(w + 0);
+    ushort_t* X2TH    = (ushort_t*)(w + 0);
+    ushort_t* X2TL    = (ushort_t*)(w + 16 * MB);
+    ushort_t* A3H     = (ushort_t*)(w + 0);
+    ushort_t* A3L     = (ushort_t*)(w + 8 * MB);
+    float*    ADJ2IND = (float*)(w + 16 * MB);
+    ushort_t* ADJ2H   = (ushort_t*)(w + 24 * MB);
+    ushort_t* ADJ2L   = (ushort_t*)(w + 28 * MB);
+    ushort_t* BNH1H   = (ushort_t*)(w + 32 * MB);
+    ushort_t* BNH1L   = (ushort_t*)(w + 48 * MB);
+    ushort_t* H2TH    = (ushort_t*)(w + 32 * MB);
+    ushort_t* H2TL    = (ushort_t*)(w + 48 * MB);
+    float*    H1      = (float*)(w + 64 * MB);
+    ushort_t* ADJ1H   = (ushort_t*)(w + 64 * MB);
+    ushort_t* ADJ1L   = (ushort_t*)(w + 80 * MB);
+    ushort_t* X3TH    = (ushort_t*)(w + 64 * MB);
+    ushort_t* X3TL    = (ushort_t*)(w + 72 * MB);
+    float*    H3      = (float*)(w + 80 * MB);
+    int*   CSR    = (int*)(w + 96 * MB);
+    int*   INDEG  = (int*)(w + 100 * MB);
     int*   RSTART = INDEG + 65536;
     int*   CURSOR = RSTART + 65536;
     float* DINV   = (float*)(CURSOR + 65536);
-    float* SCORE  = (float*)(w + 73 * MB);
-    float* H1   = (float*)(w + 76 * MB);
-    float* H2   = H1;
-    float* ADJ2 = (float*)(w + 108 * MB);
-    uint8_t* mp = w + 116 * MB;
+    float* SCORE  = (float*)(w + 101 * MB);
+    uint8_t* mp = w + 101 * MB + 256 * 1024;
     int*   RANK   = (int*)mp;   mp += 256 * 1024;
     int*   IDX1   = (int*)mp;   mp += 128 * 1024;
     int*   IDX2   = (int*)mp;   mp += 64 * 1024;
@@ -677,8 +759,12 @@
     float* X1R    = (float*)mp; mp += 256 * 1024;
     float* X2R    = (float*)mp; mp += 256 * 1024;
     float* X3R    = (float*)mp; mp += 256 * 1024;
-    ushort_t* WHI = (ushort_t*)mp; mp += 256 * 1024;
-    ushort_t* WLO = (ushort_t*)mp; mp += 256 * 1024;
+    ushort_t* W1TH = (ushort_t*)mp; mp += 256 * 1024;
+    ushort_t* W1TL = (ushort_t*)mp; mp += 256 * 1024;
+    ushort_t* W2TH = (ushort_t*)mp; mp += 128 * 1024;
+    ushort_t* W2TL = (ushort_t*)mp; mp += 128 * 1024;
+    ushort_t* W3TH = (ushort_t*)mp; mp += 128 * 1024;
+    ushort_t* W3TL = (ushort_t*)mp; mp += 128 * 1024;
 
     float* Hout = OUT + OFF_XU;
 
@@ -687,8 +773,12 @@
     hipMemsetAsync(SC2, 0, 128 * 1024, stream);
     hipMemsetAsync(X1R, 0, 768 * 1024, stream);
 
-    split_w_kernel<<<512, 256, 0, stream>>>(W1, WHI, WLO);
-    gemm_xw_mfma<<<dim3(512, 2), 256, 0, stream>>>(X, WHI, WLO, XWp);
+    bn_kernel<<<1, 256, 0, stream>>>(GAM, BET, MEA, VAR, SBN, TBN);
+    split_wT_kernel<<<512, 256, 0, stream>>>(W1, 512, W1TH, W1TL);
+    split_wT_kernel<<<256, 256, 0, stream>>>(W2, 256, W2TH, W2TL);
+    split_wT_kernel<<<256, 256, 0, stream>>>(W3, 256, W3TH, W3TL);
+
+    gemm_xw_mfma<<<dim3(512, 2), 256, 0, stream>>>(X, W1TH, W1TL, XWp);
     count_kernel<<<4096, 256, 0, stream>>>(dst, INDEG);
     scan_kernel<<<1, 1024, 0, stream>>>(INDEG, RSTART, CURSOR);
     scatter_csr_kernel<<<4096, 256, 0, stream>>>(src, dst, CURSOR, CSR);
@@ -697,25 +787,28 @@
                                                 CSR, B1v, (float4*)Hout);
     score_kernel<<<16384, 256, 0, stream>>>((const float4*)Hout, RSTART, INDEG, CSR, SCORE);
     topk_kernel<<<128, 512, 0, stream>>>(SCORE, 512, 256, IDX1, RANK, 512);
-    gather_rows_kernel<<<32768, 64, 0, stream>>>((const float4*)Hout, IDX1, 256, 512, (float4*)H1);
+    gather_bn_kernel<<<32768, 64, 0, stream>>>((const float4*)Hout, IDX1, SBN, TBN,
+                                               (float4*)H1, BNH1H, BNH1L);
     readout_kernel<<<dim3(128, 4), 256, 0, stream>>>(H1, 256, X1R);
     ef_plain_kernel<<<8192, 256, 0, stream>>>((const float4*)H1, ATT1, E1, F1);
-    hipMemsetAsync(ADJ1, 0, (size_t)32 * MB, stream);
-    scatter_A_kernel<<<4096, 256, 0, stream>>>(src, dst, RANK, ADJ1);
-    softmax_adj_kernel<<<32768, 256, 0, stream>>>(ADJ1, E1, F1, 256);
-    rowsum_kernel<<<8192, 256, 0, stream>>>(ADJ1, 256, RS1, DV1);
-    bn_kernel<<<1, 256, 0, stream>>>(GAM, BET, MEA, VAR, SBN, TBN);
-    gemm_x2_kernel<<<dim3(4, 4, 128), 256, 0, stream>>>(H1, W2, SBN, TBN, DV1, X2);
-    gemm_h2_kernel<<<dim3(4, 4, 128), 256, 0, stream>>>(ADJ1, X2, DV1, B2v, H2);
-    gemm_score_kernel<<<dim3(4, 4, 128), 256, 0, stream>>>(ADJ1, H2, RS1, SC2);
+    hipMemsetAsync(IND1, 0, (size_t)32 * MB, stream);
+    scatter_A_kernel<<<4096, 256, 0, stream>>>(src, dst, RANK, IND1);
+    softmax_split_kernel<<<32768, 256, 0, stream>>>(IND1, E1, F1, 256, ADJ1H, ADJ1L);
+    rowsum_split_kernel<<<8192, 256, 0, stream>>>(ADJ1H, ADJ1L, 256, RS1, DV1);
+    gemm_x2_mfma<<<dim3(2, 2, 128), 256, 0, stream>>>(BNH1H, BNH1L, W2TH, W2TL, DV1,
+                                                      X2TH, X2TL);
+    gemm_h2_mfma<<<dim3(2, 2, 128), 256, 0, stream>>>(ADJ1H, ADJ1L, X2TH, X2TL, DV1, B2v,
+                                                      H2TH, H2TL);
+    gemm_score_mfma<<<dim3(2, 2, 128), 256, 0, stream>>>(ADJ1H, ADJ1L, H2TH, H2TL, RS1, SC2);
     topk_kernel<<<128, 256, 0, stream>>>(SC2, 256, 128, IDX2, nullptr, 0);
-    readout_idx_kernel<<<dim3(128, 4), 256, 0, stream>>>(H2, IDX2, 128, 256, X2R);
-    ef_idx_kernel<<<4096, 256, 0, stream>>>((const float4*)H2, IDX2, 128, 256, ATT2, E2, F2);
-    gather_adj2_kernel<<<dim3(128, 128), 128, 0, stream>>>(ADJ1, IDX2, ADJ2);
-    softmax_adj_kernel<<<16384, 128, 0, stream>>>(ADJ2, E2, F2, 128);
-    rowsum_kernel<<<4096, 256, 0, stream>>>(ADJ2, 128, RS2, DV2);
-    gemm_x3_kernel<<<dim3(2, 4, 128), 256, 0, stream>>>(H2, IDX2, W3, DV2, X3);
-    gemm_h3_kernel<<<dim3(2, 4, 128), 256, 0, stream>>>(ADJ2, X3, DV2, B3v, H3);
+    gather_a3_kernel<<<16384, 64, 0, stream>>>(H2TH, H2TL, IDX2, A3H, A3L);
+    readout_split_kernel<<<dim3(128, 4), 256, 0, stream>>>(A3H, A3L, 128, X2R);
+    ef_split_kernel<<<4096, 256, 0, stream>>>(A3H, A3L, ATT2, E2, F2);
+    gather_adj2_split_kernel<<<dim3(128, 128), 128, 0, stream>>>(ADJ1H, ADJ1L, IDX2, ADJ2IND);
+    softmax_split_kernel<<<16384, 128, 0, stream>>>(ADJ2IND, E2, F2, 128, ADJ2H, ADJ2L);
+    rowsum_split_kernel<<<4096, 256, 0, stream>>>(ADJ2H, ADJ2L, 128, RS2, DV2);
+    gemm_x3_mfma<<<dim3(1, 2, 128), 256, 0, stream>>>(A3H, A3L, W3TH, W3TL, DV2, X3TH, X3TL);
+    gemm_h3_mfma<<<dim3(1, 2, 128), 256, 0, stream>>>(ADJ2H, ADJ2L, X3TH, X3TL, DV2, B3v, H3);
     readout_kernel<<<dim3(128, 4), 256, 0, stream>>>(H3, 128, X3R);
     head_kernel<<<128, 256, 0, stream>>>(X1R, X2R, X3R, L1W, L1B, L2W, L2B, L3W, L3B,
                                          OUT, OUT + OFF_LOGP);
```

After: 1.026 ms. 1.02x faster.
